# Kernel optimization log

Measured on AMD Instinct MI355X. Metric: run time of the kernel, lower is better.

Reference implementation:

```python
import jax, jax.numpy as jnp
import numpy as np

N_CLUSTERS = 64
COLLAPSE_REG = 0.1
H_SMOOTH = -0.0001
H_ALPHA = 0.0001
H_LAMBDA = 0.0001


def setup_inputs() -> dict:
    key = jax.random.key(0)
    ks = jax.random.split(key, 6)
    n, d, k = 65536, 512, N_CLUSTERS
    e0 = 1048576  # directed edges before symmetrization
    features = jax.random.normal(ks[0], (n, d), jnp.float32)
    s = jax.random.randint(ks[1], (e0,), 0, n)
    t = jax.random.randint(ks[2], (e0,), 0, n)
    v = jax.random.uniform(ks[3], (e0,), jnp.float32)
    # symmetrize adjacency (real graph datasets are undirected -> L = D - A is PSD)
    edge_src = jnp.concatenate([s, t]).astype(jnp.int64)
    edge_dst = jnp.concatenate([t, s]).astype(jnp.int64)
    edge_vals = jnp.concatenate([v, v])
    W = jax.random.normal(ks[4], (d, k), jnp.float32) / np.sqrt(d).astype(np.float32)
    b = jnp.zeros((k,), jnp.float32)
    return dict(features=features, edge_src=edge_src, edge_dst=edge_dst,
                edge_vals=edge_vals, W=W, b=b)


def reference(features, edge_src, edge_dst, edge_vals, W, b):
    n, d = features.shape
    k = W.shape[1]
    # assignments = softmax(Dense(features))
    S = jax.nn.softmax(features @ W + b, axis=1)  # [n,k]
    cluster_sizes = jnp.sum(S, axis=0)            # [k]
    S_pool = S / cluster_sizes                    # [n,k]
    # sparse column-degree (tf.sparse.reduce_sum axis=0) and edge count
    deg_col = jax.ops.segment_sum(edge_vals, edge_dst, num_segments=n)[:, None]  # [n,1]
    m = jnp.sum(deg_col)
    # A @ S via edge-list gather/scatter (sparse_dense_matmul)
    AS = jax.ops.segment_sum(edge_vals[:, None] * S[edge_dst], edge_src,
                             num_segments=n)      # [n,k]
    graph_pooled = AS.T @ S                       # S^T A S, [k,k]
    normalizer = ((S.T @ deg_col) @ (deg_col.T @ S)) / 2.0 / m  # [k,k]
    spectral_loss = -jnp.trace(graph_pooled - normalizer) / 2.0 / m
    collapse_loss = (jnp.linalg.norm(cluster_sizes) / n
                     * jnp.sqrt(jnp.float32(k)) - 1.0)
    # pooled features
    FP = jax.nn.selu(S_pool.T @ features)         # [k,d]
    # FGC loss chain: Laplacian L = D_row - A applied sparsely
    deg_row = jax.ops.segment_sum(edge_vals, edge_src, num_segments=n)[:, None]
    LS = deg_row * S - AS                         # L @ S, [n,k]
    StLS = LS.T @ S                               # smoothness1 = S^T L S, [k,k]
    # log(det(StLS + ones)) computed stably via slogdet (det is positive: PSD + rank-1)
    _sign, logabsdet = jnp.linalg.slogdet(StLS + jnp.ones_like(StLS))
    smoothness_loss = logabsdet * H_SMOOTH
    # trace((L S) @ FP @ FP^T): trace of [n,k] matrix = sum of first k diagonal entries
    trace_loss = jnp.einsum('ic,cd,id->', LS[:k], FP, FP)
    frob_loss = jnp.linalg.norm(S @ FP - features) * H_ALPHA
    one_two_loss = jnp.linalg.norm(jnp.sum(jnp.abs(S), axis=0)) * H_LAMBDA
    fgc_loss = smoothness_loss + trace_loss + frob_loss + one_two_loss
    total_loss = spectral_loss + COLLAPSE_REG * collapse_loss + fgc_loss
    return FP, S, total_loss
```

## Files before the change

kernel.cpp:

```cpp
#include <hip/hip_runtime.h>
#include <hip/hip_bf16.h>
#include <cstdint>
#include <cstddef>

typedef unsigned short u16;
typedef float f32x4 __attribute__((ext_vector_type(4)));
typedef short bf16x8 __attribute__((ext_vector_type(8)));
typedef unsigned short u16x8 __attribute__((ext_vector_type(8)));

__device__ __forceinline__ u16 f2bf(float f) {
    uint32_t u = __float_as_uint(f);
    u += 0x7fffu + ((u >> 16) & 1u);
    return (u16)(u >> 16);
}
__device__ __forceinline__ float bf2f(u16 h) {
    return __uint_as_float(((uint32_t)h) << 16);
}

#define SWZ(c) ((((c) ^ ((c) >> 3)) & 7) << 2)

__global__ __launch_bounds__(256) void k_prep(const float* __restrict__ Wg, u16* __restrict__ Wt) {
    int idx = blockIdx.x * 256 + threadIdx.x;
    int k = idx >> 6, c = idx & 63;
    int lin = c * 512 + (k ^ ((c & 7) << 3));
    Wt[lin] = f2bf(Wg[idx]);
}

__global__ __launch_bounds__(256) void k1(const float* __restrict__ F,
    const u16* __restrict__ WtG, const float* __restrict__ bias,
    float* __restrict__ S_out, u16* __restrict__ Sbf,
    float* __restrict__ sizes, float* __restrict__ scal) {
    __shared__ __align__(16) u16 Wl[64 * 512];
    __shared__ __align__(16) u16 Al[64 * 64];
    __shared__ float red4[4];
    const int tid = threadIdx.x;
    const int row0 = blockIdx.x * 64;
    for (int j = tid; j < 4096; j += 256)
        ((uint4*)Wl)[j] = ((const uint4*)WtG)[j];

    const int lane = tid & 63;
    const int wv = __builtin_amdgcn_readfirstlane(tid >> 6);
    const int l15 = lane & 15, lq = lane >> 4;
    f32x4 acc[4];
    #pragma unroll
    for (int tn = 0; tn < 4; tn++)
        #pragma unroll
        for (int e = 0; e < 4; e++) acc[tn][e] = 0.f;
    float sumf2 = 0.f;
    const int sr = tid >> 2, skq = tid & 3;
    const int sw = (sr & 7) << 3;

    for (int k0 = 0; k0 < 512; k0 += 64) {
        const float* fp = F + (size_t)(row0 + sr) * 512 + k0 + skq * 16;
        float4 v[4];
        u16 h[16];
        #pragma unroll
        for (int q = 0; q < 4; q++) v[q] = ((const float4*)fp)[q];
        #pragma unroll
        for (int q = 0; q < 4; q++) {
            sumf2 += v[q].x * v[q].x + v[q].y * v[q].y + v[q].z * v[q].z + v[q].w * v[q].w;
            h[q * 4 + 0] = f2bf(v[q].x); h[q * 4 + 1] = f2bf(v[q].y);
            h[q * 4 + 2] = f2bf(v[q].z); h[q * 4 + 3] = f2bf(v[q].w);
        }
        #pragma unroll
        for (int half = 0; half < 2; half++) {
            u16x8 pk;
            #pragma unroll
            for (int e2 = 0; e2 < 8; e2++) pk[e2] = h[half * 8 + e2];
            *(u16x8*)&Al[sr * 64 + ((skq * 16 + half * 8) ^ sw)] = pk;
        }
        __syncthreads();
        #pragma unroll
        for (int kk = 0; kk < 64; kk += 32) {
            const int arow = wv * 16 + l15;
            bf16x8 a = *(const bf16x8*)&Al[arow * 64 + ((kk + lq * 8) ^ ((arow & 7) << 3))];
            #pragma unroll
            for (int tn = 0; tn < 4; tn++) {
                const int bc = tn * 16 + l15;
                bf16x8 b = *(const bf16x8*)&Wl[bc * 512 + ((k0 + kk + lq * 8) ^ ((bc & 7) << 3))];
                acc[tn] = __builtin_amdgcn_mfma_f32_16x16x32_bf16(a, b, acc[tn], 0, 0, 0);
            }
        }
        __syncthreads();
    }

    float bias4[4], szacc[4] = {0.f, 0.f, 0.f, 0.f};
    #pragma unroll
    for (int tn = 0; tn < 4; tn++) bias4[tn] = bias[tn * 16 + l15];
    #pragma unroll
    for (int r2 = 0; r2 < 4; r2++) {
        float L[4];
        #pragma unroll
        for (int tn = 0; tn < 4; tn++) L[tn] = acc[tn][r2] + bias4[tn];
        float mx = fmaxf(fmaxf(L[0], L[1]), fmaxf(L[2], L[3]));
        #pragma unroll
        for (int mm = 1; mm < 16; mm <<= 1) mx = fmaxf(mx, __shfl_xor(mx, mm));
        float e[4], s = 0.f;
        #pragma unroll
        for (int tn = 0; tn < 4; tn++) { e[tn] = __expf(L[tn] - mx); s += e[tn]; }
        #pragma unroll
        for (int mm = 1; mm < 16; mm <<= 1) s += __shfl_xor(s, mm);
        const float inv = 1.f / s;
        const size_t grow = (size_t)(row0 + wv * 16 + lq * 4 + r2);
        #pragma unroll
        for (int tn = 0; tn < 4; tn++) {
            const float svl = e[tn] * inv;
            S_out[grow * 64 + tn * 16 + l15] = svl;
            Sbf[grow * 64 + tn * 16 + l15] = f2bf(svl);
            szacc[tn] += svl;
        }
    }
    #pragma unroll
    for (int tn = 0; tn < 4; tn++) {
        float vs = szacc[tn];
        vs += __shfl_xor(vs, 16);
        vs += __shfl_xor(vs, 32);
        if (lq == 0) atomicAdd(sizes + tn * 16 + l15, vs);
    }
    #pragma unroll
    for (int mm = 1; mm < 64; mm <<= 1) sumf2 += __shfl_xor(sumf2, mm);
    if (lane == 0) red4[wv] = sumf2;
    __syncthreads();
    if (tid == 0) atomicAdd(scal + 1, red4[0] + red4[1] + red4[2] + red4[3]);
}

__global__ __launch_bounds__(512) void k_sweep(const int* __restrict__ esrc,
    const int* __restrict__ edst, const float* __restrict__ ev,
    const u16* __restrict__ Sbf, const float* __restrict__ S, const int E2,
    float* __restrict__ GP8, float* __restrict__ SDS8, float* __restrict__ u8,
    float* __restrict__ AS64, float* __restrict__ deg64, float* __restrict__ scal) {
    __shared__ uint32_t Tl[2][2048];
    __shared__ uint32_t Pl[2][2048];
    __shared__ uint32_t Ql[2][2048];
    __shared__ uint32_t Rl[2][2048];
    const int tid = threadIdx.x;
    const int lane = tid & 63;
    const int wv = __builtin_amdgcn_readfirstlane(tid >> 6);
    const int l15 = lane & 15, lq = lane >> 4;
    const int xcd = blockIdx.x & 7;
    float* __restrict__ GPmy = GP8 + (size_t)xcd * 4096;
    float* __restrict__ SDSmy = SDS8 + (size_t)xcd * 4096;
    float* __restrict__ umy = u8 + (size_t)xcd * 64;

    const bool isP = tid < 256;
    const int st = tid & 255;
    const int p = st >> 3, g = st & 7;
    float vsum = 0.f;
    float uacc[8];
    #pragma unroll
    for (int j = 0; j < 8; j++) uacc[j] = 0.f;

    f32x4 aG[2], aS[2];
    #pragma unroll
    for (int t = 0; t < 2; t++)
        #pragma unroll
        for (int r = 0; r < 4; r++) { aG[t][r] = 0.f; aS[t][r] = 0.f; }

    const int ma = 16 * (wv & 3) + l15;
    const int aoff = ma * 32, aswz = SWZ(ma);
    const int nb0 = 32 * (wv >> 2) + l15;
    const int nb1 = nb0 + 16;
    const int b0off = nb0 * 32, b0swz = SWZ(nb0);
    const int b1off = nb1 * 32, b1swz = SWZ(nb1);

    const int nch = E2 >> 6;
    const int stride = gridDim.x;
    int ch = blockIdx.x;
    if (ch >= nch) return;

    int2 ia_c, ib_c, ia_n, ib_n;
    float2 vv_c, vv_n;
    {
        const int e0 = (ch << 6) + 2 * p;
        ia_c = isP ? *(const int2*)&edst[e0] : *(const int2*)&esrc[e0];
        ib_c = isP ? *(const int2*)&esrc[e0] : *(const int2*)&edst[e0];
        vv_c = *(const float2*)&ev[e0];
    }
    u16x8 ra_c = *(const u16x8*)&Sbf[(size_t)ia_c.x * 64 + 8 * g];
    u16x8 rb_c = *(const u16x8*)&Sbf[(size_t)ia_c.y * 64 + 8 * g];
    int chn = ch + stride;
    {
        const int chc = chn < nch ? chn : (nch - 1);
        const int e0 = (chc << 6) + 2 * p;
        ia_n = isP ? *(const int2*)&edst[e0] : *(const int2*)&esrc[e0];
        ib_n = isP ? *(const int2*)&esrc[e0] : *(const int2*)&edst[e0];
        vv_n = *(const float2*)&ev[e0];
    }

    int buf = 0;
    while (true) {
        if (isP) {
            #pragma unroll
            for (int j = 0; j < 8; j++) {
                const int c = 8 * g + j;
                const int off = c * 32 + (p ^ SWZ(c));
                Tl[buf][off] = (uint32_t)(u16)ra_c[j] | ((uint32_t)(u16)rb_c[j] << 16);
                Pl[buf][off] = (uint32_t)f2bf(vv_c.x * bf2f((u16)ra_c[j])) |
                               ((uint32_t)f2bf(vv_c.y * bf2f((u16)rb_c[j])) << 16);
            }
        } else {
            #pragma unroll
            for (int j = 0; j < 8; j++) {
                const int c = 8 * g + j;
                const int off = c * 32 + (p ^ SWZ(c));
                Ql[buf][off] = (uint32_t)(u16)ra_c[j] | ((uint32_t)(u16)rb_c[j] << 16);
                Rl[buf][off] = (uint32_t)f2bf(vv_c.x * bf2f((u16)ra_c[j])) |
                               ((uint32_t)f2bf(vv_c.y * bf2f((u16)rb_c[j])) << 16);
            }
        }
        #pragma unroll
        for (int j = 0; j < 8; j++)
            uacc[j] = fmaf(vv_c.x, bf2f((u16)ra_c[j]),
                      fmaf(vv_c.y, bf2f((u16)rb_c[j]), uacc[j]));
        if (!isP && g == 0) vsum += vv_c.x + vv_c.y;
        if (g == 0) {
            if (ib_c.x < 64) atomicAdd(deg64 + ib_c.x, vv_c.x);
            if (ib_c.y < 64) atomicAdd(deg64 + ib_c.y, vv_c.y);
        }
        if (ib_c.x < 64) {
            const float4 fa = *(const float4*)(S + (size_t)ia_c.x * 64 + 8 * g);
            const float4 fb = *(const float4*)(S + (size_t)ia_c.x * 64 + 8 * g + 4);
            float* dst = AS64 + ib_c.x * 64 + 8 * g;
            atomicAdd(dst + 0, vv_c.x * fa.x); atomicAdd(dst + 1, vv_c.x * fa.y);
            atomicAdd(dst + 2, vv_c.x * fa.z); atomicAdd(dst + 3, vv_c.x * fa.w);
            atomicAdd(dst + 4, vv_c.x * fb.x); atomicAdd(dst + 5, vv_c.x * fb.y);
            atomicAdd(dst + 6, vv_c.x * fb.z); atomicAdd(dst + 7, vv_c.x * fb.w);
        }
        if (ib_c.y < 64) {
            const float4 fa = *(const float4*)(S + (size_t)ia_c.y * 64 + 8 * g);
            const float4 fb = *(const float4*)(S + (size_t)ia_c.y * 64 + 8 * g + 4);
            float* dst = AS64 + ib_c.y * 64 + 8 * g;
            atomicAdd(dst + 0, vv_c.y * fa.x); atomicAdd(dst + 1, vv_c.y * fa.y);
            atomicAdd(dst + 2, vv_c.y * fa.z); atomicAdd(dst + 3, vv_c.y * fa.w);
            atomicAdd(dst + 4, vv_c.y * fb.x); atomicAdd(dst + 5, vv_c.y * fb.y);
            atomicAdd(dst + 6, vv_c.y * fb.z); atomicAdd(dst + 7, vv_c.y * fb.w);
        }
        const u16x8 ra_n = *(const u16x8*)&Sbf[(size_t)ia_n.x * 64 + 8 * g];
        const u16x8 rb_n = *(const u16x8*)&Sbf[(size_t)ia_n.y * 64 + 8 * g];
        const int chnn = chn + stride;
        int2 ia_nn, ib_nn;
        float2 vv_nn;
        {
            const int chc = chnn < nch ? chnn : (nch - 1);
            const int e0 = (chc << 6) + 2 * p;
            ia_nn = isP ? *(const int2*)&edst[e0] : *(const int2*)&esrc[e0];
            ib_nn = isP ? *(const int2*)&esrc[e0] : *(const int2*)&edst[e0];
            vv_nn = *(const float2*)&ev[e0];
        }
        __syncthreads();
        #pragma unroll
        for (int half = 0; half < 2; half++) {
            const int w0 = half * 16 + lq * 4;
            const bf16x8 afP = *(const bf16x8*)&Pl[buf][aoff + (w0 ^ aswz)];
            const bf16x8 afR = *(const bf16x8*)&Rl[buf][aoff + (w0 ^ aswz)];
            const bf16x8 qb0 = *(const bf16x8*)&Ql[buf][b0off + (w0 ^ b0swz)];
            const bf16x8 qb1 = *(const bf16x8*)&Ql[buf][b1off + (w0 ^ b1swz)];
            const bf16x8 tb0 = *(const bf16x8*)&Tl[buf][b0off + (w0 ^ b0swz)];
            const bf16x8 tb1 = *(const bf16x8*)&Tl[buf][b1off + (w0 ^ b1swz)];
            aG[0] = __builtin_amdgcn_mfma_f32_16x16x32_bf16(afP, qb0, aG[0], 0, 0, 0);
            aG[1] = __builtin_amdgcn_mfma_f32_16x16x32_bf16(afP, qb1, aG[1], 0, 0, 0);
            aS[0] = __builtin_amdgcn_mfma_f32_16x16x32_bf16(afR, qb0, aS[0], 0, 0, 0);
            aS[1] = __builtin_amdgcn_mfma_f32_16x16x32_bf16(afR, qb1, aS[1], 0, 0, 0);
            aS[0] = __builtin_amdgcn_mfma_f32_16x16x32_bf16(afP, tb0, aS[0], 0, 0, 0);
            aS[1] = __builtin_amdgcn_mfma_f32_16x16x32_bf16(afP, tb1, aS[1], 0, 0, 0);
        }
        ch = chn;
        if (ch >= nch) break;
        ia_c = ia_n; ib_c = ib_n; vv_c = vv_n; ra_c = ra_n; rb_c = rb_n;
        ia_n = ia_nn; ib_n = ib_nn; vv_n = vv_nn;
        chn = chnn;
        buf ^= 1;
    }
    #pragma unroll
    for (int t = 0; t < 2; t++)
        #pragma unroll
        for (int r = 0; r < 4; r++) {
            const int c1 = 16 * (wv & 3) + 4 * lq + r;
            const int c2 = 32 * (wv >> 2) + 16 * t + l15;
            atomicAdd(GPmy + c1 * 64 + c2, aG[t][r]);
            atomicAdd(SDSmy + c1 * 64 + c2, aS[t][r]);
        }
    #pragma unroll
    for (int j = 0; j < 8; j++) {
        uacc[j] += __shfl_xor(uacc[j], 8);
        uacc[j] += __shfl_xor(uacc[j], 16);
        uacc[j] += __shfl_xor(uacc[j], 32);
    }
    if (lane < 8) {
        #pragma unroll
        for (int j = 0; j < 8; j++)
            atomicAdd(umy + 8 * lane + j, uacc[j]);
    }
    if (wv >= 4) {
        #pragma unroll
        for (int mm = 1; mm < 64; mm <<= 1) vsum += __shfl_xor(vsum, mm);
        if (lane == 0) atomicAdd(scal + 0, vsum + vsum);
    }
}

__global__ __launch_bounds__(256) void k_mrg(const float* __restrict__ GP8,
    const float* __restrict__ SDS8, const float* __restrict__ u8,
    float* __restrict__ GP, float* __restrict__ SDS, float* __restrict__ u_vec) {
    const int bid = blockIdx.x;
    const int t = threadIdx.x;
    if (bid < 16) {
        const int j = bid * 256 + t;
        const int jt = (j & 63) * 64 + (j >> 6);
        float s = 0.f;
        #pragma unroll
        for (int c = 0; c < 8; c++)
            s += GP8[(size_t)c * 4096 + j] + GP8[(size_t)c * 4096 + jt];
        GP[j] = s;
    } else if (bid < 32) {
        const int j = (bid - 16) * 256 + t;
        float s = 0.f;
        #pragma unroll
        for (int c = 0; c < 8; c++) s += SDS8[(size_t)c * 4096 + j];
        SDS[j] = s;
    } else if (t < 64) {
        float s = 0.f;
        #pragma unroll
        for (int c = 0; c < 8; c++) s += u8[c * 64 + t];
        u_vec[t] = s;
    }
}

__global__ __launch_bounds__(256) void k2m(const float* __restrict__ F,
    const u16* __restrict__ Sbf, float* __restrict__ G) {
    __shared__ uint32_t Ss[64 * 32];
    __shared__ uint32_t Fs[128 * 32];
    const int tid = threadIdx.x;
    const int lane = tid & 63;
    const int wv = __builtin_amdgcn_readfirstlane(tid >> 6);
    const int l15 = lane & 15, lq = lane >> 4;
    const int d0 = (blockIdx.x & 3) * 128;
    const int kblk = blockIdx.x >> 2;

    f32x4 acc[8];
    #pragma unroll
    for (int t8 = 0; t8 < 8; t8++)
        #pragma unroll
        for (int r = 0; r < 4; r++) acc[t8][r] = 0.f;

    const int s_ip = tid >> 3;
    const int s_cs = (tid & 7) * 8;
    const int f_dg = tid & 31;
    const int f_ipb = tid >> 5;

    for (int ch = 0; ch < 8; ch++) {
        const int i0 = kblk * 512 + ch * 64;
        {
            const u16x8 r0 = *(const u16x8*)&Sbf[(size_t)(i0 + 2 * s_ip) * 64 + s_cs];
            const u16x8 r1 = *(const u16x8*)&Sbf[(size_t)(i0 + 2 * s_ip + 1) * 64 + s_cs];
            #pragma unroll
            for (int j = 0; j < 8; j++) {
                const int c = s_cs + j;
                const uint32_t pk = (uint32_t)(u16)r0[j] | ((uint32_t)(u16)r1[j] << 16);
                Ss[c * 32 + (s_ip ^ (((c >> 2) & 7) << 2))] = pk;
            }
        }
        #pragma unroll
        for (int s = 0; s < 4; s++) {
            const int ip = f_ipb + 8 * s;
            const float4 a = *(const float4*)(F + (size_t)(i0 + 2 * ip) * 512 + d0 + 4 * f_dg);
            const float4 b = *(const float4*)(F + (size_t)(i0 + 2 * ip + 1) * 512 + d0 + 4 * f_dg);
            const float al[4] = {a.x, a.y, a.z, a.w};
            const float bl[4] = {b.x, b.y, b.z, b.w};
            #pragma unroll
            for (int j = 0; j < 4; j++) {
                const int d = 4 * f_dg + j;
                const uint32_t pk = (uint32_t)f2bf(al[j]) | ((uint32_t)f2bf(bl[j]) << 16);
                Fs[d * 32 + (ip ^ (((d >> 2) & 7) << 2))] = pk;
            }
        }
        __syncthreads();
        #pragma unroll
        for (int kk = 0; kk < 64; kk += 32) {
            const int w0 = (kk >> 1) + (lq << 2);
            const int ca = 16 * wv + l15;
            const bf16x8 afrag = *(const bf16x8*)&Ss[ca * 32 + (w0 ^ (((ca >> 2) & 7) << 2))];
            #pragma unroll
            for (int t8 = 0; t8 < 8; t8++) {
                const int d = 16 * t8 + l15;
                const bf16x8 bfrag = *(const bf16x8*)&Fs[d * 32 + (w0 ^ (((d >> 2) & 7) << 2))];
                acc[t8] = __builtin_amdgcn_mfma_f32_16x16x32_bf16(afrag, bfrag, acc[t8], 0, 0, 0);
            }
        }
        __syncthreads();
    }
    #pragma unroll
    for (int t8 = 0; t8 < 8; t8++) {
        #pragma unroll
        for (int r = 0; r < 4; r++) {
            const int c = 16 * wv + 4 * lq + r;
            const int d = d0 + 16 * t8 + l15;
            atomicAdd(G + (size_t)c * 512 + d, acc[t8][r]);
        }
    }
}

__global__ __launch_bounds__(256) void k_kk(const u16* __restrict__ Sbf,
    float* __restrict__ SS) {
    __shared__ float Pss[4][16][64];
    const int tid = threadIdx.x, lane = tid & 63;
    const int wv = __builtin_amdgcn_readfirstlane(tid >> 6);
    const int cs = blockIdx.x & 3, c0 = cs * 16;
    const int rbase = (blockIdx.x >> 2) * 512 + wv * 128;
    float ss[16];
    #pragma unroll
    for (int cc = 0; cc < 16; cc++) ss[cc] = 0.f;
    for (int r = 0; r < 128; r++) {
        const int i = rbase + r;
        const float sv = bf2f(Sbf[(size_t)i * 64 + lane]);
        const u16* srow = Sbf + (size_t)i * 64 + c0;
        #pragma unroll
        for (int cc = 0; cc < 16; cc++)
            ss[cc] = fmaf(bf2f(srow[cc]), sv, ss[cc]);
    }
    #pragma unroll
    for (int cc = 0; cc < 16; cc++) Pss[wv][cc][lane] = ss[cc];
    __syncthreads();
    for (int q = 0; q < 4; q++) {
        const int cell = tid * 4 + q, cc = cell >> 6, l = cell & 63;
        atomicAdd(SS + (c0 + cc) * 64 + l,
                  Pss[0][cc][l] + Pss[1][cc][l] + Pss[2][cc][l] + Pss[3][cc][l]);
    }
}

__device__ __forceinline__ float bred256(float v, float* red) {
    #pragma unroll
    for (int mm = 1; mm < 64; mm <<= 1) v += __shfl_xor(v, mm);
    const int t = threadIdx.x;
    __syncthreads();
    if ((t & 63) == 0) red[t >> 6] = v;
    __syncthreads();
    return red[0] + red[1] + red[2] + red[3];
}

__global__ __launch_bounds__(256) void k_fp(const float* __restrict__ G,
    const float* __restrict__ sizes, float* __restrict__ FP, float* __restrict__ scal) {
    __shared__ float red[4];
    const int idx = blockIdx.x * 256 + threadIdx.x;
    const int c = idx >> 9;
    const float g = G[idx];
    const float x = g / sizes[c];
    const float fp = 1.0507009873554805f * (x > 0.f ? x : 1.6732632423543772f * (__expf(x) - 1.f));
    FP[idx] = fp;
    const float gd = bred256(g * fp, red);
    if (threadIdx.x == 0) atomicAdd(scal + 2, gd);
}

__global__ __launch_bounds__(256) void k_fft(const float* __restrict__ FP, float* __restrict__ FFt) {
    __shared__ float red[256];
    const int c = blockIdx.x;
    const int cp = threadIdx.x & 63, part = threadIdx.x >> 6;
    float a = 0.f;
    const int dbase = part * 128;
    for (int dd = 0; dd < 128; dd++)
        a = fmaf(FP[c * 512 + dbase + dd], FP[cp * 512 + dbase + dd], a);
    red[threadIdx.x] = a;
    __syncthreads();
    if (threadIdx.x < 64)
        FFt[c * 64 + threadIdx.x] = red[threadIdx.x] + red[threadIdx.x + 64] +
                                    red[threadIdx.x + 128] + red[threadIdx.x + 192];
}

__global__ __launch_bounds__(64) void k_lu(const float* __restrict__ SDS,
    const float* __restrict__ GP, float* __restrict__ scal) {
    __shared__ float M[64][65];
    const int l = threadIdx.x;
    for (int c = 0; c < 64; c++) M[l][c] = SDS[l * 64 + c] - GP[l * 64 + c] + 1.0f;
    __syncthreads();
    float logdet = 0.f;
    for (int k = 0; k < 64; k++) {
        float v = (l >= k) ? fabsf(M[l][k]) : -1.f;
        int idx = l;
        #pragma unroll
        for (int mm = 1; mm < 64; mm <<= 1) {
            const float ov = __shfl_xor(v, mm);
            const int oi = __shfl_xor(idx, mm);
            if (ov > v || (ov == v && oi < idx)) { v = ov; idx = oi; }
        }
        if (idx != k) {
            const float t1 = M[k][l], t2 = M[idx][l];
            __syncthreads();
            M[k][l] = t2;
            M[idx][l] = t1;
        }
        __syncthreads();
        const float piv = M[k][k];
        logdet += logf(fabsf(piv));
        if (l > k) {
            const float f = M[l][k] / piv;
            for (int c = k + 1; c < 64; c++) M[l][c] = fmaf(-f, M[k][c], M[l][c]);
        }
        __syncthreads();
    }
    if (l == 0) scal[3] = logdet;
}

__global__ __launch_bounds__(256) void k_final(const float* __restrict__ GP,
    const float* __restrict__ SS, const float* __restrict__ FFt, const float* __restrict__ u_vec,
    const float* __restrict__ sizes, const float* __restrict__ deg64,
    const float* __restrict__ AS64, const float* __restrict__ S,
    const float* __restrict__ scal, float* __restrict__ out_loss, const float fn) {
    __shared__ float red[4];
    const int t = threadIdx.x;
    float sA = 0.f, trl = 0.f, trg = 0.f, u2 = 0.f, sz2 = 0.f;
    for (int q = t; q < 4096; q += 256) sA += SS[q] * FFt[q];
    for (int q = t; q < 4096; q += 256) {
        const int i = q >> 6, c = q & 63;
        const float ls = deg64[i] * S[i * 64 + c] - AS64[q];
        trl += ls * FFt[c * 64 + i];
    }
    if (t < 64) { trg = GP[t * 65]; u2 = u_vec[t] * u_vec[t]; sz2 = sizes[t] * sizes[t]; }
    sA = bred256(sA, red);
    trl = bred256(trl, red);
    trg = bred256(trg, red);
    u2 = bred256(u2, red);
    sz2 = bred256(sz2, red);
    if (t == 0) {
        const float m = scal[0], sumF2 = scal[1], gfp = scal[2], lad = scal[3];
        const float spectral = -(trg - u2 / (2.f * m)) / (2.f * m);
        const float collapse = sqrtf(sz2) / fn * 8.f - 1.f;
        const float frob = sqrtf(fmaxf(sA - 2.f * gfp + sumF2, 0.f)) * 1e-4f;
        const float one_two = sqrtf(sz2) * 1e-4f;
        const float smooth = lad * (-1e-4f);
        out_loss[0] = spectral + 0.1f * collapse + smooth + trl + frob + one_two;
    }
}

extern "C" void kernel_launch(void* const* d_in, const int* in_sizes, int n_in,
                              void* d_out, int out_size, void* d_ws, size_t ws_size,
                              hipStream_t stream) {
    const float* F = (const float*)d_in[0];
    const int* esrc = (const int*)d_in[1];
    const int* edst = (const int*)d_in[2];
    const float* ev = (const float*)d_in[3];
    const float* Wg = (const float*)d_in[4];
    const float* bg = (const float*)d_in[5];
    const int n = in_sizes[0] / 512;
    const int E = in_sizes[1];
    const int E2 = E >> 1;

    float* outF = (float*)d_out;
    float* outS = outF + 64 * 512;
    float* outL = outS + (size_t)n * 64;

    char* w = (char*)d_ws;
    float* sizes = (float*)w;
    float* u_vec = sizes + 64;
    float* scal = u_vec + 64;
    float* G = scal + 64;
    float* SS = G + 64 * 512;
    float* AS64 = SS + 4096;
    float* deg64 = AS64 + 4096;
    float* GP8 = deg64 + 64;
    float* SDS8 = GP8 + 8 * 4096;
    float* u8 = SDS8 + 8 * 4096;
    char* zend = (char*)(u8 + 512);
    const size_t zero_bytes = (size_t)(zend - w);
    float* GP = (float*)zend;
    float* SDS = GP + 4096;
    float* FFt = SDS + 4096;
    u16* Sbf = (u16*)(FFt + 4096);
    u16* Wt = Sbf + (size_t)n * 64;

    hipMemsetAsync(d_ws, 0, zero_bytes, stream);
    k_prep<<<128, 256, 0, stream>>>(Wg, Wt);
    k1<<<n / 64, 256, 0, stream>>>(F, Wt, bg, outS, Sbf, sizes, scal);
    k_sweep<<<512, 512, 0, stream>>>(esrc, edst, ev, Sbf, outS, E2, GP8, SDS8, u8, AS64, deg64, scal);
    k2m<<<512, 256, 0, stream>>>(F, Sbf, G);
    k_mrg<<<33, 256, 0, stream>>>(GP8, SDS8, u8, GP, SDS, u_vec);
    k_kk<<<(n / 512) * 4, 256, 0, stream>>>(Sbf, SS);
    k_fp<<<128, 256, 0, stream>>>(G, sizes, outF, scal);
    k_fft<<<64, 256, 0, stream>>>(outF, FFt);
    k_lu<<<1, 64, 0, stream>>>(SDS, GP, scal);
    k_final<<<1, 256, 0, stream>>>(GP, SS, FFt, u_vec, sizes, deg64, AS64, outS, scal, outL, (float)n);
}
```

Measured before the change: 526.9 us.

## Quantize S to int8 for edge sweep and use int8 MFMA

Adds an int8 copy of the soft assignments (scaled by 127) written in k1. The edge sweep now gathers int8 rows, builds int8 LDS tiles with a new padded swizzle, and accumulates S^T A S terms with i32 MFMA before rescaling to float. The sweep grid also doubles to 1024 blocks. The aim is to halve gather bandwidth and LDS traffic in the sweep. The cost is much coarser precision: edge-weighted products are rounded to int8, which may hurt loss accuracy, and k1 does an extra store.

```diff
diff --git a/kernel.cpp b/kernel.cpp
--- a/kernel.cpp
+++ b/kernel.cpp
@@ -4,9 +4,12 @@
 #include <cstddef>
 
 typedef unsigned short u16;
+typedef unsigned char u8;
 typedef float f32x4 __attribute__((ext_vector_type(4)));
+typedef int i32x4 __attribute__((ext_vector_type(4)));
 typedef short bf16x8 __attribute__((ext_vector_type(8)));
 typedef unsigned short u16x8 __attribute__((ext_vector_type(8)));
+typedef signed char i8x8 __attribute__((ext_vector_type(8)));
 
 __device__ __forceinline__ u16 f2bf(float f) {
     uint32_t u = __float_as_uint(f);
@@ -17,7 +20,7 @@
     return __uint_as_float(((uint32_t)h) << 16);
 }
 
-#define SWZ(c) ((((c) ^ ((c) >> 3)) & 7) << 2)
+#define LD8(tile, row, u) (*(const long*)&(tile)[(row) * 72 + 8 * ((u) ^ (((row) >> 3) & 7))])
 
 __global__ __launch_bounds__(256) void k_prep(const float* __restrict__ Wg, u16* __restrict__ Wt) {
     int idx = blockIdx.x * 256 + threadIdx.x;
@@ -28,7 +31,7 @@
 
 __global__ __launch_bounds__(256) void k1(const float* __restrict__ F,
     const u16* __restrict__ WtG, const float* __restrict__ bias,
-    float* __restrict__ S_out, u16* __restrict__ Sbf,
+    float* __restrict__ S_out, u16* __restrict__ Sbf, signed char* __restrict__ Sq,
     float* __restrict__ sizes, float* __restrict__ scal) {
     __shared__ __align__(16) u16 Wl[64 * 512];
     __shared__ __align__(16) u16 Al[64 * 64];
@@ -107,6 +110,7 @@
             const float svl = e[tn] * inv;
             S_out[grow * 64 + tn * 16 + l15] = svl;
             Sbf[grow * 64 + tn * 16 + l15] = f2bf(svl);
+            Sq[grow * 64 + tn * 16 + l15] = (signed char)(int)(svl * 127.f + 0.5f);
             szacc[tn] += svl;
         }
     }
@@ -126,13 +130,13 @@
 
 __global__ __launch_bounds__(512) void k_sweep(const int* __restrict__ esrc,
     const int* __restrict__ edst, const float* __restrict__ ev,
-    const u16* __restrict__ Sbf, const float* __restrict__ S, const int E2,
-    float* __restrict__ GP8, float* __restrict__ SDS8, float* __restrict__ u8,
+    const signed char* __restrict__ Sq, const float* __restrict__ S, const int E2,
+    float* __restrict__ GP8, float* __restrict__ SDS8, float* __restrict__ uv8,
     float* __restrict__ AS64, float* __restrict__ deg64, float* __restrict__ scal) {
-    __shared__ uint32_t Tl[2][2048];
-    __shared__ uint32_t Pl[2][2048];
-    __shared__ uint32_t Ql[2][2048];
-    __shared__ uint32_t Rl[2][2048];
+    __shared__ signed char Tq[2][64 * 72];
+    __shared__ signed char Pq[2][64 * 72];
+    __shared__ signed char Qq[2][64 * 72];
+    __shared__ signed char Rq[2][64 * 72];
     const int tid = threadIdx.x;
     const int lane = tid & 63;
     const int wv = __builtin_amdgcn_readfirstlane(tid >> 6);
@@ -140,28 +144,27 @@
     const int xcd = blockIdx.x & 7;
     float* __restrict__ GPmy = GP8 + (size_t)xcd * 4096;
     float* __restrict__ SDSmy = SDS8 + (size_t)xcd * 4096;
-    float* __restrict__ umy = u8 + (size_t)xcd * 64;
+    float* __restrict__ umy = uv8 + (size_t)xcd * 64;
 
     const bool isP = tid < 256;
     const int st = tid & 255;
     const int p = st >> 3, g = st & 7;
+    const int ub = p >> 2;
+    const int bo = 2 * (p & 3);
     float vsum = 0.f;
     float uacc[8];
     #pragma unroll
     for (int j = 0; j < 8; j++) uacc[j] = 0.f;
 
-    f32x4 aG[2], aS[2];
+    i32x4 aG[2], aS[2];
     #pragma unroll
     for (int t = 0; t < 2; t++)
         #pragma unroll
-        for (int r = 0; r < 4; r++) { aG[t][r] = 0.f; aS[t][r] = 0.f; }
+        for (int r = 0; r < 4; r++) { aG[t][r] = 0; aS[t][r] = 0; }
 
     const int ma = 16 * (wv & 3) + l15;
-    const int aoff = ma * 32, aswz = SWZ(ma);
     const int nb0 = 32 * (wv >> 2) + l15;
     const int nb1 = nb0 + 16;
-    const int b0off = nb0 * 32, b0swz = SWZ(nb0);
-    const int b1off = nb1 * 32, b1swz = SWZ(nb1);
 
     const int nch = E2 >> 6;
     const int stride = gridDim.x;
@@ -176,8 +179,8 @@
         ib_c = isP ? *(const int2*)&esrc[e0] : *(const int2*)&edst[e0];
         vv_c = *(const float2*)&ev[e0];
     }
-    u16x8 ra_c = *(const u16x8*)&Sbf[(size_t)ia_c.x * 64 + 8 * g];
-    u16x8 rb_c = *(const u16x8*)&Sbf[(size_t)ia_c.y * 64 + 8 * g];
+    i8x8 ra_c = *(const i8x8*)&Sq[(size_t)ia_c.x * 64 + 8 * g];
+    i8x8 rb_c = *(const i8x8*)&Sq[(size_t)ia_c.y * 64 + 8 * g];
     int chn = ch + stride;
     {
         const int chc = chn < nch ? chn : (nch - 1);
@@ -193,25 +196,29 @@
             #pragma unroll
             for (int j = 0; j < 8; j++) {
                 const int c = 8 * g + j;
-                const int off = c * 32 + (p ^ SWZ(c));
-                Tl[buf][off] = (uint32_t)(u16)ra_c[j] | ((uint32_t)(u16)rb_c[j] << 16);
-                Pl[buf][off] = (uint32_t)f2bf(vv_c.x * bf2f((u16)ra_c[j])) |
-                               ((uint32_t)f2bf(vv_c.y * bf2f((u16)rb_c[j])) << 16);
+                const int off = c * 72 + 8 * (ub ^ ((c >> 3) & 7)) + bo;
+                const int qa = (int)ra_c[j], qb = (int)rb_c[j];
+                *(u16*)&Tq[buf][off] = (u16)(((u16)(u8)qa) | ((u16)(u8)qb << 8));
+                const int pa = (int)(vv_c.x * (float)qa + 0.5f);
+                const int pb = (int)(vv_c.y * (float)qb + 0.5f);
+                *(u16*)&Pq[buf][off] = (u16)(((u16)(u8)pa) | ((u16)(u8)pb << 8));
             }
         } else {
             #pragma unroll
             for (int j = 0; j < 8; j++) {
                 const int c = 8 * g + j;
-                const int off = c * 32 + (p ^ SWZ(c));
-                Ql[buf][off] = (uint32_t)(u16)ra_c[j] | ((uint32_t)(u16)rb_c[j] << 16);
-                Rl[buf][off] = (uint32_t)f2bf(vv_c.x * bf2f((u16)ra_c[j])) |
-                               ((uint32_t)f2bf(vv_c.y * bf2f((u16)rb_c[j])) << 16);
+                const int off = c * 72 + 8 * (ub ^ ((c >> 3) & 7)) + bo;
+                const int qa = (int)ra_c[j], qb = (int)rb_c[j];
+                *(u16*)&Qq[buf][off] = (u16)(((u16)(u8)qa) | ((u16)(u8)qb << 8));
+                const int pa = (int)(vv_c.x * (float)qa + 0.5f);
+                const int pb = (int)(vv_c.y * (float)qb + 0.5f);
+                *(u16*)&Rq[buf][off] = (u16)(((u16)(u8)pa) | ((u16)(u8)pb << 8));
             }
         }
         #pragma unroll
         for (int j = 0; j < 8; j++)
-            uacc[j] = fmaf(vv_c.x, bf2f((u16)ra_c[j]),
-                      fmaf(vv_c.y, bf2f((u16)rb_c[j]), uacc[j]));
+            uacc[j] = fmaf(vv_c.x, (float)ra_c[j],
+                      fmaf(vv_c.y, (float)rb_c[j], uacc[j]));
         if (!isP && g == 0) vsum += vv_c.x + vv_c.y;
         if (g == 0) {
             if (ib_c.x < 64) atomicAdd(deg64 + ib_c.x, vv_c.x);
@@ -235,8 +242,8 @@
             atomicAdd(dst + 4, vv_c.y * fb.x); atomicAdd(dst + 5, vv_c.y * fb.y);
             atomicAdd(dst + 6, vv_c.y * fb.z); atomicAdd(dst + 7, vv_c.y * fb.w);
         }
-        const u16x8 ra_n = *(const u16x8*)&Sbf[(size_t)ia_n.x * 64 + 8 * g];
-        const u16x8 rb_n = *(const u16x8*)&Sbf[(size_t)ia_n.y * 64 + 8 * g];
+        const i8x8 ra_n = *(const i8x8*)&Sq[(size_t)ia_n.x * 64 + 8 * g];
+        const i8x8 rb_n = *(const i8x8*)&Sq[(size_t)ia_n.y * 64 + 8 * g];
         const int chnn = chn + stride;
         int2 ia_nn, ib_nn;
         float2 vv_nn;
@@ -250,19 +257,19 @@
         __syncthreads();
         #pragma unroll
         for (int half = 0; half < 2; half++) {
-            const int w0 = half * 16 + lq * 4;
-            const bf16x8 afP = *(const bf16x8*)&Pl[buf][aoff + (w0 ^ aswz)];
-            const bf16x8 afR = *(const bf16x8*)&Rl[buf][aoff + (w0 ^ aswz)];
-            const bf16x8 qb0 = *(const bf16x8*)&Ql[buf][b0off + (w0 ^ b0swz)];
-            const bf16x8 qb1 = *(const bf16x8*)&Ql[buf][b1off + (w0 ^ b1swz)];
-            const bf16x8 tb0 = *(const bf16x8*)&Tl[buf][b0off + (w0 ^ b0swz)];
-            const bf16x8 tb1 = *(const bf16x8*)&Tl[buf][b1off + (w0 ^ b1swz)];
-            aG[0] = __builtin_amdgcn_mfma_f32_16x16x32_bf16(afP, qb0, aG[0], 0, 0, 0);
-            aG[1] = __builtin_amdgcn_mfma_f32_16x16x32_bf16(afP, qb1, aG[1], 0, 0, 0);
-            aS[0] = __builtin_amdgcn_mfma_f32_16x16x32_bf16(afR, qb0, aS[0], 0, 0, 0);
-            aS[1] = __builtin_amdgcn_mfma_f32_16x16x32_bf16(afR, qb1, aS[1], 0, 0, 0);
-            aS[0] = __builtin_amdgcn_mfma_f32_16x16x32_bf16(afP, tb0, aS[0], 0, 0, 0);
-            aS[1] = __builtin_amdgcn_mfma_f32_16x16x32_bf16(afP, tb1, aS[1], 0, 0, 0);
+            const int uA = half * 4 + lq;
+            const long aP = LD8(Pq[buf], ma, uA);
+            const long aR = LD8(Rq[buf], ma, uA);
+            const long bQ0 = LD8(Qq[buf], nb0, uA);
+            const long bQ1 = LD8(Qq[buf], nb1, uA);
+            const long bT0 = LD8(Tq[buf], nb0, uA);
+            const long bT1 = LD8(Tq[buf], nb1, uA);
+            aG[0] = __builtin_amdgcn_mfma_i32_16x16x32_i8(aP, bQ0, aG[0], 0, 0, 0);
+            aG[1] = __builtin_amdgcn_mfma_i32_16x16x32_i8(aP, bQ1, aG[1], 0, 0, 0);
+            aS[0] = __builtin_amdgcn_mfma_i32_16x16x32_i8(aR, bQ0, aS[0], 0, 0, 0);
+            aS[1] = __builtin_amdgcn_mfma_i32_16x16x32_i8(aR, bQ1, aS[1], 0, 0, 0);
+            aS[0] = __builtin_amdgcn_mfma_i32_16x16x32_i8(aP, bT0, aS[0], 0, 0, 0);
+            aS[1] = __builtin_amdgcn_mfma_i32_16x16x32_i8(aP, bT1, aS[1], 0, 0, 0);
         }
         ch = chn;
         if (ch >= nch) break;
@@ -271,14 +278,15 @@
         chn = chnn;
         buf ^= 1;
     }
+    const float sc = 1.f / 16129.f;
     #pragma unroll
     for (int t = 0; t < 2; t++)
         #pragma unroll
         for (int r = 0; r < 4; r++) {
             const int c1 = 16 * (wv & 3) + 4 * lq + r;
             const int c2 = 32 * (wv >> 2) + 16 * t + l15;
-            atomicAdd(GPmy + c1 * 64 + c2, aG[t][r]);
-            atomicAdd(SDSmy + c1 * 64 + c2, aS[t][r]);
+            atomicAdd(GPmy + c1 * 64 + c2, (float)aG[t][r] * sc);
+            atomicAdd(SDSmy + c1 * 64 + c2, (float)aS[t][r] * sc);
         }
     #pragma unroll
     for (int j = 0; j < 8; j++) {
@@ -289,7 +297,7 @@
     if (lane < 8) {
         #pragma unroll
         for (int j = 0; j < 8; j++)
-            atomicAdd(umy + 8 * lane + j, uacc[j]);
+            atomicAdd(umy + 8 * lane + j, uacc[j] * (1.f / 127.f));
     }
     if (wv >= 4) {
         #pragma unroll
@@ -299,7 +307,7 @@
 }
 
 __global__ __launch_bounds__(256) void k_mrg(const float* __restrict__ GP8,
-    const float* __restrict__ SDS8, const float* __restrict__ u8,
+    const float* __restrict__ SDS8, const float* __restrict__ uv8,
     float* __restrict__ GP, float* __restrict__ SDS, float* __restrict__ u_vec) {
     const int bid = blockIdx.x;
     const int t = threadIdx.x;
@@ -320,7 +328,7 @@
     } else if (t < 64) {
         float s = 0.f;
         #pragma unroll
-        for (int c = 0; c < 8; c++) s += u8[c * 64 + t];
+        for (int c = 0; c < 8; c++) s += uv8[c * 64 + t];
         u_vec[t] = s;
     }
 }
@@ -557,21 +565,22 @@
     float* deg64 = AS64 + 4096;
     float* GP8 = deg64 + 64;
     float* SDS8 = GP8 + 8 * 4096;
-    float* u8 = SDS8 + 8 * 4096;
-    char* zend = (char*)(u8 + 512);
+    float* u8buf = SDS8 + 8 * 4096;
+    char* zend = (char*)(u8buf + 512);
     const size_t zero_bytes = (size_t)(zend - w);
     float* GP = (float*)zend;
     float* SDS = GP + 4096;
     float* FFt = SDS + 4096;
     u16* Sbf = (u16*)(FFt + 4096);
     u16* Wt = Sbf + (size_t)n * 64;
+    signed char* Sq = (signed char*)(Wt + 64 * 512);
 
     hipMemsetAsync(d_ws, 0, zero_bytes, stream);
     k_prep<<<128, 256, 0, stream>>>(Wg, Wt);
-    k1<<<n / 64, 256, 0, stream>>>(F, Wt, bg, outS, Sbf, sizes, scal);
-    k_sweep<<<512, 512, 0, stream>>>(esrc, edst, ev, Sbf, outS, E2, GP8, SDS8, u8, AS64, deg64, scal);
+    k1<<<n / 64, 256, 0, stream>>>(F, Wt, bg, outS, Sbf, Sq, sizes, scal);
+    k_sweep<<<1024, 512, 0, stream>>>(esrc, edst, ev, Sq, outS, E2, GP8, SDS8, u8buf, AS64, deg64, scal);
     k2m<<<512, 256, 0, stream>>>(F, Sbf, G);
-    k_mrg<<<33, 256, 0, stream>>>(GP8, SDS8, u8, GP, SDS, u_vec);
+    k_mrg<<<33, 256, 0, stream>>>(GP8, SDS8, u8buf, GP, SDS, u_vec);
     k_kk<<<(n / 512) * 4, 256, 0, stream>>>(Sbf, SS);
     k_fp<<<128, 256, 0, stream>>>(G, sizes, outF, scal);
     k_fft<<<64, 256, 0, stream>>>(outF, FFt);
```

Measured after the change: 616.4 us. 17.0% more time.
